# Optimization experiments

Hardware: AMD Instinct MI355X
Metric: run time of the kernel (lower is better)

## Reference

```python
import jax, jax.numpy as jnp
import numpy as np

N_NODES = 100000
N_EDGES = 1600000
IN_CH, HID_CH, OUT_CH = 128, 128, 64


def setup_inputs() -> dict:
    key = jax.random.key(0)
    k1, k2, k3, k4 = jax.random.split(key, 4)
    x = jax.random.normal(k1, (N_NODES, IN_CH), dtype=jnp.float32)
    edge_index = jax.random.randint(k2, (2, N_EDGES), 0, N_NODES, dtype=jnp.int64)
    # Glorot-like init for the two GCNConv weight matrices, zero biases (PyG default)
    W1 = jax.random.normal(k3, (IN_CH, HID_CH), dtype=jnp.float32) * (1.0 / np.sqrt(IN_CH))
    b1 = jnp.zeros((HID_CH,), dtype=jnp.float32)
    W2 = jax.random.normal(k4, (HID_CH, OUT_CH), dtype=jnp.float32) * (1.0 / np.sqrt(HID_CH))
    b2 = jnp.zeros((OUT_CH,), dtype=jnp.float32)
    return {"x": x, "edge_index": edge_index, "W1": W1, "b1": b1, "W2": W2, "b2": b2}


def _gcn_conv(x, src, dst, norm, W, b):
    """One GCNConv: linear transform, gather normalized source messages, scatter-add."""
    h = x @ W                                  # [N, out]
    msg = h[src] * norm[:, None]               # [E+N, out] gather + scale
    out = jax.ops.segment_sum(msg, dst, num_segments=N_NODES)  # scatter-add
    return out + b


def _build_norm(edge_index):
    # add self-loops (PyG GCNConv default add_self_loops=True)
    loops = jnp.arange(N_NODES, dtype=edge_index.dtype)
    src = jnp.concatenate([edge_index[0], loops])  # message sources (x_j)
    dst = jnp.concatenate([edge_index[1], loops])  # aggregation targets
    deg = jax.ops.segment_sum(jnp.ones_like(dst, dtype=jnp.float32), dst,
                              num_segments=N_NODES)
    dinv = jnp.where(deg > 0, jax.lax.rsqrt(jnp.maximum(deg, 1.0)), 0.0)
    norm = dinv[src] * dinv[dst]               # symmetric normalization per edge
    return src, dst, norm


def reference(x, edge_index, W1, b1, W2, b2):
    src, dst, norm = _build_norm(edge_index)
    h = _gcn_conv(x, src, dst, norm, W1, b1)
    h = jax.nn.relu(h)
    out = _gcn_conv(h, src, dst, norm, W2, b2)
    return out
```

## Files before the change

kernel.cpp:

```cpp
#include <hip/hip_runtime.h>
#include <cstdint>
#include <cstddef>

#define N_NODES 100000
#define N_EDGES 1600000
#define IN_CH   128
#define HID_CH  128
#define OUT_CH  64

#define AGG_BLOCKS 2048

#define SH    256
#define SHR   391
#define BCAP  7200
#define BK_CHUNK 4096
#define BK_NBLK ((N_EDGES + BK_CHUNK - 1) / BK_CHUNK)

__device__ __forceinline__ unsigned short f2bf(float f) {
    unsigned int u = __float_as_uint(f);
    unsigned int r = (u + 0x7FFFu + ((u >> 16) & 1u)) >> 16;
    return (unsigned short)r;
}
__device__ __forceinline__ float bfbits2f(unsigned int lo16) {
    return __uint_as_float(lo16 << 16);
}

typedef __attribute__((ext_vector_type(8))) short bf16x8;
typedef __attribute__((ext_vector_type(4))) float f32x4;

__global__ __launch_bounds__(512) void k_bucket(const int* __restrict__ ei,
                                                int* __restrict__ gcur,
                                                long long* __restrict__ buckets) {
    __shared__ int scount[8][SH];
    __shared__ int sbase[8][SH];
    const int tid  = threadIdx.x;
    const int w    = tid >> 6;
    const int base = blockIdx.x * BK_CHUNK;
    for (int i = tid; i < 8 * SH; i += 512) ((int*)scount)[i] = 0;
    __syncthreads();
    int dv[8], sv[8], shd[8], rk[8];
    #pragma unroll
    for (int k = 0; k < 8; k++) {
        int e = base + k * 512 + tid;
        if (e < N_EDGES) {
            dv[k] = __builtin_nontemporal_load(ei + N_EDGES + e);
            sv[k] = __builtin_nontemporal_load(ei + e);
            shd[k] = dv[k] / SHR;
            rk[k] = atomicAdd(&scount[w][shd[k]], 1);
        } else shd[k] = -1;
    }
    __syncthreads();
    if (tid < SH) {
        int c[8], tot = 0;
        #pragma unroll
        for (int q = 0; q < 8; q++) { c[q] = scount[q][tid]; tot += c[q]; }
        int run = atomicAdd(&gcur[tid], tot);
        #pragma unroll
        for (int q = 0; q < 8; q++) { sbase[q][tid] = run; run += c[q]; }
    }
    __syncthreads();
    #pragma unroll
    for (int k = 0; k < 8; k++) {
        if (shd[k] >= 0) {
            int pos = sbase[w][shd[k]] + rk[k];
            if (pos < BCAP)
                buckets[(size_t)shd[k] * BCAP + pos] =
                    ((long long)sv[k] << 32) | (unsigned int)dv[k];
        }
    }
}

__global__ __launch_bounds__(1024) void k_build(const long long* __restrict__ buckets,
                                                const int* __restrict__ gcur,
                                                int* __restrict__ rowptr,
                                                float* __restrict__ dinv,
                                                int* __restrict__ srcs) {
    __shared__ int hist[SHR];
    __shared__ int pref[SH];
    __shared__ int wsum[16];
    const int s  = blockIdx.x;
    const int lo = s * SHR;
    const int nb = min(SHR, N_NODES - lo);
    const int n  = min(gcur[s], BCAP);
    const int t = threadIdx.x, lane = t & 63, wid = t >> 6;
    const long long* bp = buckets + (size_t)s * BCAP;

    if (t < SH) pref[t] = gcur[t];
    for (int i = t; i < SHR; i += 1024) hist[i] = 0;
    __syncthreads();
    if (wid == 0) {
        int v0 = pref[lane * 4], v1 = pref[lane * 4 + 1];
        int v2 = pref[lane * 4 + 2], v3 = pref[lane * 4 + 3];
        int sl = v0 + v1 + v2 + v3;
        int x = sl;
        #pragma unroll
        for (int d = 1; d < 64; d <<= 1) {
            int y = __shfl_up(x, d, 64);
            if (lane >= d) x += y;
        }
        int excl = x - sl;
        pref[lane * 4]     = excl;
        pref[lane * 4 + 1] = excl + v0;
        pref[lane * 4 + 2] = excl + v0 + v1;
        pref[lane * 4 + 3] = excl + v0 + v1 + v2;
        if (s == 0 && lane == 63) rowptr[N_NODES] = x;
    }
    __syncthreads();
    const int gbase = pref[s];

    for (int i = t; i < n; i += 1024) {
        atomicAdd(&hist[(int)bp[i] - lo], 1);
    }
    __syncthreads();

    {
        int idx = t;
        int v = (idx < SHR) ? hist[idx] : 0;
        int x = v;
        #pragma unroll
        for (int d = 1; d < 64; d <<= 1) {
            int y = __shfl_up(x, d, 64);
            if (lane >= d) x += y;
        }
        if (lane == 63) wsum[wid] = x;
        __syncthreads();
        if (wid == 0) {
            int sv = (lane < 16) ? wsum[lane] : 0;
            #pragma unroll
            for (int d = 1; d < 16; d <<= 1) {
                int y = __shfl_up(sv, d, 64);
                if (lane >= d) sv += y;
            }
            if (lane < 16) wsum[lane] = sv;
        }
        __syncthreads();
        int woff = (wid == 0) ? 0 : wsum[wid - 1];
        int excl = woff + (x - v);
        if (idx < nb) {
            rowptr[lo + idx] = gbase + excl;
            dinv[lo + idx]   = rsqrtf((float)(v + 1));
        }
        if (idx < SHR) hist[idx] = excl;
        __syncthreads();
    }

    for (int i = t; i < n; i += 1024) {
        long long v = bp[i];
        int d  = (int)v;
        int sv = (int)(v >> 32);
        int pos = atomicAdd(&hist[d - lo], 1);
        srcs[gbase + pos] = sv;
    }
}

template <int OC>
__global__ __launch_bounds__(256) void k_gemm_mfma(const float* __restrict__ A,
                                                   const float* __restrict__ W,
                                                   unsigned short* __restrict__ hb) {
    __shared__ unsigned short As[128 * 128];
    __shared__ unsigned short Ws[OC * 128];
    const int tid = threadIdx.x;
    const int l   = tid & 63;
    const int wv  = tid >> 6;
    const int row0 = blockIdx.x * 128;

    #pragma unroll
    for (int it = 0; it < 16; it++) {
        int idx4 = it * 256 + tid;
        int r = idx4 >> 5, c4 = idx4 & 31;
        int gr = row0 + r; if (gr >= N_NODES) gr = N_NODES - 1;
        float4 v = ((const float4*)(A + (size_t)gr * 128))[c4];
        int bi = (r * 128 + c4 * 4) ^ ((r & 7) << 3);
        ushort4 pk;
        pk.x = f2bf(v.x); pk.y = f2bf(v.y); pk.z = f2bf(v.z); pk.w = f2bf(v.w);
        *(ushort4*)&As[bi] = pk;
    }
    for (int idx = tid; idx < 128 * OC; idx += 256) {
        int k = idx / OC, c = idx % OC;
        Ws[(c * 128 + k) ^ ((c & 7) << 3)] = f2bf(W[idx]);
    }
    __syncthreads();

    constexpr int NCF = OC / 16;
    f32x4 acc[2][NCF];
    #pragma unroll
    for (int a = 0; a < 2; a++)
        #pragma unroll
        for (int b = 0; b < NCF; b++) acc[a][b] = {0.f, 0.f, 0.f, 0.f};

    const int fr = l & 15;
    const int kg = (l >> 4) * 8;

    #pragma unroll
    for (int ks = 0; ks < 4; ks++) {
        const int kk = ks * 32 + kg;
        bf16x8 a0, a1;
        {
            int r = wv * 32 + fr;
            a0 = *(const bf16x8*)&As[(r * 128 + kk) ^ ((r & 7) << 3)];
            r += 16;
            a1 = *(const bf16x8*)&As[(r * 128 + kk) ^ ((r & 7) << 3)];
        }
        #pragma unroll
        for (int cf = 0; cf < NCF; cf++) {
            int c = cf * 16 + fr;
            bf16x8 b = *(const bf16x8*)&Ws[(c * 128 + kk) ^ ((c & 7) << 3)];
            acc[0][cf] = __builtin_amdgcn_mfma_f32_16x16x32_bf16(a0, b, acc[0][cf], 0, 0, 0);
            acc[1][cf] = __builtin_amdgcn_mfma_f32_16x16x32_bf16(a1, b, acc[1][cf], 0, 0, 0);
        }
    }

    const int g4 = (l >> 4) * 4;
    #pragma unroll
    for (int rf = 0; rf < 2; rf++)
        #pragma unroll
        for (int cf = 0; cf < NCF; cf++)
            #pragma unroll
            for (int r = 0; r < 4; r++) {
                int grow = row0 + wv * 32 + rf * 16 + g4 + r;
                if (grow < N_NODES)
                    hb[(size_t)grow * OC + cf * 16 + fr] = f2bf(acc[rf][cf][r]);
            }
}

template <int OC>
__global__ __launch_bounds__(256) void k_gemm_mfma_b(const unsigned short* __restrict__ A,
                                                     const float* __restrict__ W,
                                                     unsigned short* __restrict__ hb) {
    __shared__ unsigned short As[128 * 128];
    __shared__ unsigned short Ws[OC * 128];
    const int tid = threadIdx.x;
    const int l   = tid & 63;
    const int wv  = tid >> 6;
    const int row0 = blockIdx.x * 128;

    #pragma unroll
    for (int it = 0; it < 8; it++) {
        int idx8 = it * 256 + tid;
        int r = idx8 >> 4, c8 = idx8 & 15;
        int gr = row0 + r; if (gr >= N_NODES) gr = N_NODES - 1;
        uint4 v = ((const uint4*)(A + (size_t)gr * 128))[c8];
        int bi = (r * 128 + c8 * 8) ^ ((r & 7) << 3);
        *(uint4*)&As[bi] = v;
    }
    for (int idx = tid; idx < 128 * OC; idx += 256) {
        int k = idx / OC, c = idx % OC;
        Ws[(c * 128 + k) ^ ((c & 7) << 3)] = f2bf(W[idx]);
    }
    __syncthreads();

    constexpr int NCF = OC / 16;
    f32x4 acc[2][NCF];
    #pragma unroll
    for (int a = 0; a < 2; a++)
        #pragma unroll
        for (int b = 0; b < NCF; b++) acc[a][b] = {0.f, 0.f, 0.f, 0.f};

    const int fr = l & 15;
    const int kg = (l >> 4) * 8;

    #pragma unroll
    for (int ks = 0; ks < 4; ks++) {
        const int kk = ks * 32 + kg;
        bf16x8 a0, a1;
        {
            int r = wv * 32 + fr;
            a0 = *(const bf16x8*)&As[(r * 128 + kk) ^ ((r & 7) << 3)];
            r += 16;
            a1 = *(const bf16x8*)&As[(r * 128 + kk) ^ ((r & 7) << 3)];
        }
        #pragma unroll
        for (int cf = 0; cf < NCF; cf++) {
            int c = cf * 16 + fr;
            bf16x8 b = *(const bf16x8*)&Ws[(c * 128 + kk) ^ ((c & 7) << 3)];
            acc[0][cf] = __builtin_amdgcn_mfma_f32_16x16x32_bf16(a0, b, acc[0][cf], 0, 0, 0);
            acc[1][cf] = __builtin_amdgcn_mfma_f32_16x16x32_bf16(a1, b, acc[1][cf], 0, 0, 0);
        }
    }

    const int g4 = (l >> 4) * 4;
    #pragma unroll
    for (int rf = 0; rf < 2; rf++)
        #pragma unroll
        for (int cf = 0; cf < NCF; cf++)
            #pragma unroll
            for (int r = 0; r < 4; r++) {
                int grow = row0 + wv * 32 + rf * 16 + g4 + r;
                if (grow < N_NODES)
                    hb[(size_t)grow * OC + cf * 16 + fr] = f2bf(acc[rf][cf][r]);
            }
}

__global__ __launch_bounds__(256) void k_agg128bf(const unsigned int* __restrict__ hb,
                                                  const int* __restrict__ rowptr,
                                                  const int* __restrict__ srcs,
                                                  const float* __restrict__ dinv,
                                                  const float* __restrict__ bias,
                                                  unsigned int* __restrict__ outb,
                                                  int relu) {
    const int l = threadIdx.x & 63;
    const int wv0 = blockIdx.x * 4 + (threadIdx.x >> 6);
    const float2 bv = ((const float2*)bias)[l];

    for (int i = wv0; i < N_NODES; i += AGG_BLOCKS * 4) {
        const float di = dinv[i];
        unsigned int svv = hb[(size_t)i * 64 + l];
        const float sw = di * di;
        float2 acc;
        acc.x = bfbits2f(svv & 0xFFFFu) * sw;
        acc.y = bfbits2f(svv >> 16) * sw;

        const int start = rowptr[i], end = rowptr[i + 1];
        for (int b = start; b < end; b += 64) {
            const int eb = min(end - b, 64);
            int s = 0; float w = 0.f;
            if (l < eb) { s = srcs[b + l]; w = dinv[s] * di; }
            int j = 0;
            for (; j + 8 <= eb; j += 8) {
                int   si[8]; float wi[8];
                #pragma unroll
                for (int u = 0; u < 8; u++) { si[u] = __shfl(s, j + u); wi[u] = __shfl(w, j + u); }
                unsigned int v[8];
                #pragma unroll
                for (int u = 0; u < 8; u++) v[u] = hb[(size_t)si[u] * 64 + l];
                #pragma unroll
                for (int u = 0; u < 8; u++) {
                    acc.x = fmaf(bfbits2f(v[u] & 0xFFFFu), wi[u], acc.x);
                    acc.y = fmaf(bfbits2f(v[u] >> 16),     wi[u], acc.y);
                }
            }
            for (; j + 4 <= eb; j += 4) {
                int   si[4]; float wi[4];
                #pragma unroll
                for (int u = 0; u < 4; u++) { si[u] = __shfl(s, j + u); wi[u] = __shfl(w, j + u); }
                unsigned int v[4];
                #pragma unroll
                for (int u = 0; u < 4; u++) v[u] = hb[(size_t)si[u] * 64 + l];
                #pragma unroll
                for (int u = 0; u < 4; u++) {
                    acc.x = fmaf(bfbits2f(v[u] & 0xFFFFu), wi[u], acc.x);
                    acc.y = fmaf(bfbits2f(v[u] >> 16),     wi[u], acc.y);
                }
            }
            for (; j < eb; j++) {
                const int   sj = __shfl(s, j);
                const float wj = __shfl(w, j);
                unsigned int v = hb[(size_t)sj * 64 + l];
                acc.x = fmaf(bfbits2f(v & 0xFFFFu), wj, acc.x);
                acc.y = fmaf(bfbits2f(v >> 16),     wj, acc.y);
            }
        }
        acc.x += bv.x; acc.y += bv.y;
        if (relu) { acc.x = fmaxf(acc.x, 0.f); acc.y = fmaxf(acc.y, 0.f); }
        outb[(size_t)i * 64 + l] =
            (unsigned int)f2bf(acc.x) | ((unsigned int)f2bf(acc.y) << 16);
    }
}

__global__ __launch_bounds__(256) void k_agg64bf(const unsigned short* __restrict__ hb,
                                                 const int* __restrict__ rowptr,
                                                 const int* __restrict__ srcs,
                                                 const float* __restrict__ dinv,
                                                 const float* __restrict__ bias,
                                                 float* __restrict__ out,
                                                 int relu) {
    const int l = threadIdx.x & 63;
    const int wv0 = blockIdx.x * 4 + (threadIdx.x >> 6);
    const float bi = bias[l];

    for (int i = wv0; i < N_NODES; i += AGG_BLOCKS * 4) {
        const float di = dinv[i];
        float acc = bfbits2f((unsigned int)hb[(size_t)i * 64 + l]) * (di * di);

        const int start = rowptr[i], end = rowptr[i + 1];
        for (int b = start; b < end; b += 64) {
            const int eb = min(end - b, 64);
            int s = 0; float w = 0.f;
            if (l < eb) { s = srcs[b + l]; w = dinv[s] * di; }
            int j = 0;
            for (; j + 8 <= eb; j += 8) {
                int   si[8]; float wi[8];
                #pragma unroll
                for (int u = 0; u < 8; u++) { si[u] = __shfl(s, j + u); wi[u] = __shfl(w, j + u); }
                unsigned short v[8];
                #pragma unroll
                for (int u = 0; u < 8; u++) v[u] = hb[(size_t)si[u] * 64 + l];
                #pragma unroll
                for (int u = 0; u < 8; u++) acc = fmaf(bfbits2f((unsigned int)v[u]), wi[u], acc);
            }
            for (; j + 4 <= eb; j += 4) {
                int   si[4]; float wi[4];
                #pragma unroll
                for (int u = 0; u < 4; u++) { si[u] = __shfl(s, j + u); wi[u] = __shfl(w, j + u); }
                unsigned short v[4];
                #pragma unroll
                for (int u = 0; u < 4; u++) v[u] = hb[(size_t)si[u] * 64 + l];
                #pragma unroll
                for (int u = 0; u < 4; u++) acc = fmaf(bfbits2f((unsigned int)v[u]), wi[u], acc);
            }
            for (; j < eb; j++) {
                const int   sj = __shfl(s, j);
                const float wj = __shfl(w, j);
                acc = fmaf(bfbits2f((unsigned int)hb[(size_t)sj * 64 + l]), wj, acc);
            }
        }
        acc += bi;
        if (relu) acc = fmaxf(acc, 0.f);
        out[(size_t)i * 64 + l] = acc;
    }
}


extern "C" void kernel_launch(void* const* d_in, const int* in_sizes, int n_in,
                              void* d_out, int out_size, void* d_ws, size_t ws_size,
                              hipStream_t stream) {
    const float* x  = (const float*)d_in[0];
    const int*   ei = (const int*)d_in[1];
    const float* W1 = (const float*)d_in[2];
    const float* b1 = (const float*)d_in[3];
    const float* W2 = (const float*)d_in[4];
    const float* b2 = (const float*)d_in[5];
    float* out = (float*)d_out;

    char* p = (char*)d_ws;
    size_t used = 0;
    auto alloc = [&](size_t bytes) {
        void* q = (void*)p;
        size_t pad = (bytes + 255) & ~(size_t)255;
        p += pad;
        used += pad;
        return q;
    };
    int*   rowptr = (int*)alloc(sizeof(int) * (N_NODES + 1));
    float* dinv   = (float*)alloc(sizeof(float) * N_NODES);
    int*   gcur   = (int*)alloc(sizeof(int) * SH);
    int*   srcs   = (int*)alloc(sizeof(int) * N_EDGES);
    void*  regA   = alloc(sizeof(unsigned short) * (size_t)N_NODES * 128);
    long long* buckets = (long long*)regA;
    unsigned short* h1b = (unsigned short*)regA;
    unsigned int* agg1b = (unsigned int*)alloc(sizeof(unsigned int) * (size_t)N_NODES * 64);
    unsigned short* h2b = (unsigned short*)alloc(sizeof(unsigned short) * (size_t)N_NODES * 64);

    if (used > ws_size) return;

    hipMemsetAsync(gcur, 0, sizeof(int) * SH, stream);
    k_bucket<<<BK_NBLK, 512, 0, stream>>>(ei, gcur, buckets);
    k_build<<<SH, 1024, 0, stream>>>(buckets, gcur, rowptr, dinv, srcs);

    k_gemm_mfma<128><<<(N_NODES + 127) / 128, 256, 0, stream>>>(x, W1, h1b);
    k_agg128bf<<<AGG_BLOCKS, 256, 0, stream>>>((const unsigned int*)h1b, rowptr, srcs, dinv, b1, agg1b, 1);
    k_gemm_mfma_b<64><<<(N_NODES + 127) / 128, 256, 0, stream>>>((const unsigned short*)agg1b, W2, h2b);
    k_agg64bf<<<AGG_BLOCKS, 256, 0, stream>>>(h2b, rowptr, srcs, dinv, b2, out, 0);
}
```

Measured before the change: 194.4 us.

## Fuse bucketing with first GEMM and layer-1 aggregation with second GEMM

Edge bucketing and the first-layer GEMM now run as one horizontally fused launch, with block index choosing the role, so the two independent workloads overlap. Layer-1 aggregation (bias, ReLU) writes its 128-row tile straight into shared memory and feeds the second GEMM in the same block. This removes the agg1 intermediate round trip through global memory and two launches. In exchange, aggregation now uses only about 782 blocks with a fixed 32 nodes per wave instead of a 2048-block grid-stride loop, so load balance and occupancy may drop. Buckets also get their own buffer instead of aliasing h1b.

Result: slower. 276.9 us (+42.5%).

```diff
diff --git a/kernel.cpp b/kernel.cpp
--- a/kernel.cpp
+++ b/kernel.cpp
@@ -15,6 +15,7 @@
 #define BCAP  7200
 #define BK_CHUNK 4096
 #define BK_NBLK ((N_EDGES + BK_CHUNK - 1) / BK_CHUNK)
+#define GM_NBLK ((N_NODES + 127) / 128)
 
 __device__ __forceinline__ unsigned short f2bf(float f) {
     unsigned int u = __float_as_uint(f);
@@ -28,46 +29,106 @@
 typedef __attribute__((ext_vector_type(8))) short bf16x8;
 typedef __attribute__((ext_vector_type(4))) float f32x4;
 
-__global__ __launch_bounds__(512) void k_bucket(const int* __restrict__ ei,
+__global__ __launch_bounds__(512) void k_fused1(const int* __restrict__ ei,
                                                 int* __restrict__ gcur,
-                                                long long* __restrict__ buckets) {
-    __shared__ int scount[8][SH];
-    __shared__ int sbase[8][SH];
-    const int tid  = threadIdx.x;
-    const int w    = tid >> 6;
-    const int base = blockIdx.x * BK_CHUNK;
-    for (int i = tid; i < 8 * SH; i += 512) ((int*)scount)[i] = 0;
+                                                long long* __restrict__ buckets,
+                                                const float* __restrict__ A,
+                                                const float* __restrict__ W,
+                                                unsigned short* __restrict__ hb) {
+    __shared__ __align__(16) unsigned char smem[64 * 1024];
+    const int tid = threadIdx.x;
+
+    if (blockIdx.x < BK_NBLK) {
+        int (*scount)[SH] = (int(*)[SH])smem;
+        int (*sbase)[SH]  = (int(*)[SH])(smem + 8 * SH * 4);
+        const int w    = tid >> 6;
+        const int base = blockIdx.x * BK_CHUNK;
+        for (int i = tid; i < 8 * SH; i += 512) ((int*)scount)[i] = 0;
+        __syncthreads();
+        int dv[8], sv[8], shd[8], rk[8];
+        #pragma unroll
+        for (int k = 0; k < 8; k++) {
+            int e = base + k * 512 + tid;
+            if (e < N_EDGES) {
+                dv[k] = __builtin_nontemporal_load(ei + N_EDGES + e);
+                sv[k] = __builtin_nontemporal_load(ei + e);
+                shd[k] = dv[k] / SHR;
+                rk[k] = atomicAdd(&scount[w][shd[k]], 1);
+            } else shd[k] = -1;
+        }
+        __syncthreads();
+        if (tid < SH) {
+            int c[8], tot = 0;
+            #pragma unroll
+            for (int q = 0; q < 8; q++) { c[q] = scount[q][tid]; tot += c[q]; }
+            int run = atomicAdd(&gcur[tid], tot);
+            #pragma unroll
+            for (int q = 0; q < 8; q++) { sbase[q][tid] = run; run += c[q]; }
+        }
+        __syncthreads();
+        #pragma unroll
+        for (int k = 0; k < 8; k++) {
+            if (shd[k] >= 0) {
+                int pos = sbase[w][shd[k]] + rk[k];
+                if (pos < BCAP)
+                    buckets[(size_t)shd[k] * BCAP + pos] =
+                        ((long long)sv[k] << 32) | (unsigned int)dv[k];
+            }
+        }
+        return;
+    }
+
+    unsigned short* As = (unsigned short*)smem;
+    unsigned short* Ws = (unsigned short*)(smem + 32 * 1024);
+    const int l   = tid & 63;
+    const int wv  = tid >> 6;
+    const int row0 = (blockIdx.x - BK_NBLK) * 128;
+
+    #pragma unroll
+    for (int it = 0; it < 8; it++) {
+        int idx4 = it * 512 + tid;
+        int r = idx4 >> 5, c4 = idx4 & 31;
+        int gr = row0 + r; if (gr >= N_NODES) gr = N_NODES - 1;
+        float4 v = ((const float4*)(A + (size_t)gr * 128))[c4];
+        int bi = (r * 128 + c4 * 4) ^ ((r & 7) << 3);
+        ushort4 pk;
+        pk.x = f2bf(v.x); pk.y = f2bf(v.y); pk.z = f2bf(v.z); pk.w = f2bf(v.w);
+        *(ushort4*)&As[bi] = pk;
+    }
+    for (int idx = tid; idx < 128 * 128; idx += 512) {
+        int k = idx >> 7, c = idx & 127;
+        Ws[(c * 128 + k) ^ ((c & 7) << 3)] = f2bf(W[idx]);
+    }
     __syncthreads();
-    int dv[8], sv[8], shd[8], rk[8];
-    #pragma unroll
-    for (int k = 0; k < 8; k++) {
-        int e = base + k * 512 + tid;
-        if (e < N_EDGES) {
-            dv[k] = __builtin_nontemporal_load(ei + N_EDGES + e);
-            sv[k] = __builtin_nontemporal_load(ei + e);
-            shd[k] = dv[k] / SHR;
-            rk[k] = atomicAdd(&scount[w][shd[k]], 1);
-        } else shd[k] = -1;
-    }
-    __syncthreads();
-    if (tid < SH) {
-        int c[8], tot = 0;
-        #pragma unroll
-        for (int q = 0; q < 8; q++) { c[q] = scount[q][tid]; tot += c[q]; }
-        int run = atomicAdd(&gcur[tid], tot);
-        #pragma unroll
-        for (int q = 0; q < 8; q++) { sbase[q][tid] = run; run += c[q]; }
-    }
-    __syncthreads();
-    #pragma unroll
-    for (int k = 0; k < 8; k++) {
-        if (shd[k] >= 0) {
-            int pos = sbase[w][shd[k]] + rk[k];
-            if (pos < BCAP)
-                buckets[(size_t)shd[k] * BCAP + pos] =
-                    ((long long)sv[k] << 32) | (unsigned int)dv[k];
-        }
-    }
+
+    f32x4 acc[8];
+    #pragma unroll
+    for (int cf = 0; cf < 8; cf++) acc[cf] = {0.f, 0.f, 0.f, 0.f};
+    const int fr = l & 15;
+    const int kg = (l >> 4) * 8;
+
+    #pragma unroll
+    for (int ks = 0; ks < 4; ks++) {
+        const int kk = ks * 32 + kg;
+        int r = wv * 16 + fr;
+        bf16x8 a0 = *(const bf16x8*)&As[(r * 128 + kk) ^ ((r & 7) << 3)];
+        #pragma unroll
+        for (int cf = 0; cf < 8; cf++) {
+            int c = cf * 16 + fr;
+            bf16x8 b = *(const bf16x8*)&Ws[(c * 128 + kk) ^ ((c & 7) << 3)];
+            acc[cf] = __builtin_amdgcn_mfma_f32_16x16x32_bf16(a0, b, acc[cf], 0, 0, 0);
+        }
+    }
+
+    const int g4 = (l >> 4) * 4;
+    #pragma unroll
+    for (int cf = 0; cf < 8; cf++)
+        #pragma unroll
+        for (int r = 0; r < 4; r++) {
+            int grow = row0 + wv * 16 + g4 + r;
+            if (grow < N_NODES)
+                hb[(size_t)grow * 128 + cf * 16 + fr] = f2bf(acc[cf][r]);
+        }
 }
 
 __global__ __launch_bounds__(1024) void k_build(const long long* __restrict__ buckets,
@@ -153,44 +214,95 @@
     }
 }
 
-template <int OC>
-__global__ __launch_bounds__(256) void k_gemm_mfma(const float* __restrict__ A,
-                                                   const float* __restrict__ W,
-                                                   unsigned short* __restrict__ hb) {
-    __shared__ unsigned short As[128 * 128];
-    __shared__ unsigned short Ws[OC * 128];
+__global__ __launch_bounds__(256) void k_aggemm(const unsigned int* __restrict__ hb,
+                                                const int* __restrict__ rowptr,
+                                                const int* __restrict__ srcs,
+                                                const float* __restrict__ dinv,
+                                                const float* __restrict__ bias,
+                                                const float* __restrict__ W,
+                                                unsigned short* __restrict__ h2b) {
+    __shared__ __align__(16) unsigned char smem[48 * 1024];
+    unsigned short* As = (unsigned short*)smem;
+    unsigned short* Ws = (unsigned short*)(smem + 32 * 1024);
     const int tid = threadIdx.x;
     const int l   = tid & 63;
     const int wv  = tid >> 6;
     const int row0 = blockIdx.x * 128;
-
-    #pragma unroll
-    for (int it = 0; it < 16; it++) {
-        int idx4 = it * 256 + tid;
-        int r = idx4 >> 5, c4 = idx4 & 31;
-        int gr = row0 + r; if (gr >= N_NODES) gr = N_NODES - 1;
-        float4 v = ((const float4*)(A + (size_t)gr * 128))[c4];
-        int bi = (r * 128 + c4 * 4) ^ ((r & 7) << 3);
-        ushort4 pk;
-        pk.x = f2bf(v.x); pk.y = f2bf(v.y); pk.z = f2bf(v.z); pk.w = f2bf(v.w);
-        *(ushort4*)&As[bi] = pk;
-    }
-    for (int idx = tid; idx < 128 * OC; idx += 256) {
-        int k = idx / OC, c = idx % OC;
+    const float2 bv = ((const float2*)bias)[l];
+
+    for (int idx = tid; idx < 128 * 64; idx += 256) {
+        int k = idx >> 6, c = idx & 63;
         Ws[(c * 128 + k) ^ ((c & 7) << 3)] = f2bf(W[idx]);
     }
+
+    for (int t = 0; t < 32; t++) {
+        const int i = row0 + wv * 32 + t;
+        float2 acc = {0.f, 0.f};
+        if (i < N_NODES) {
+            const float di = dinv[i];
+            unsigned int svv = hb[(size_t)i * 64 + l];
+            const float sw = di * di;
+            acc.x = bfbits2f(svv & 0xFFFFu) * sw;
+            acc.y = bfbits2f(svv >> 16) * sw;
+
+            const int start = rowptr[i], end = rowptr[i + 1];
+            for (int b = start; b < end; b += 64) {
+                const int eb = min(end - b, 64);
+                int s = 0; float w = 0.f;
+                if (l < eb) { s = srcs[b + l]; w = dinv[s] * di; }
+                int j = 0;
+                for (; j + 8 <= eb; j += 8) {
+                    int   si[8]; float wi[8];
+                    #pragma unroll
+                    for (int u = 0; u < 8; u++) { si[u] = __shfl(s, j + u); wi[u] = __shfl(w, j + u); }
+                    unsigned int v[8];
+                    #pragma unroll
+                    for (int u = 0; u < 8; u++) v[u] = hb[(size_t)si[u] * 64 + l];
+                    #pragma unroll
+                    for (int u = 0; u < 8; u++) {
+                        acc.x = fmaf(bfbits2f(v[u] & 0xFFFFu), wi[u], acc.x);
+                        acc.y = fmaf(bfbits2f(v[u] >> 16),     wi[u], acc.y);
+                    }
+                }
+                for (; j + 4 <= eb; j += 4) {
+                    int   si[4]; float wi[4];
+                    #pragma unroll
+                    for (int u = 0; u < 4; u++) { si[u] = __shfl(s, j + u); wi[u] = __shfl(w, j + u); }
+                    unsigned int v[4];
+                    #pragma unroll
+                    for (int u = 0; u < 4; u++) v[u] = hb[(size_t)si[u] * 64 + l];
+                    #pragma unroll
+                    for (int u = 0; u < 4; u++) {
+                        acc.x = fmaf(bfbits2f(v[u] & 0xFFFFu), wi[u], acc.x);
+                        acc.y = fmaf(bfbits2f(v[u] >> 16),     wi[u], acc.y);
+                    }
+                }
+                for (; j < eb; j++) {
+                    const int   sj = __shfl(s, j);
+                    const float wj = __shfl(w, j);
+                    unsigned int v = hb[(size_t)sj * 64 + l];
+                    acc.x = fmaf(bfbits2f(v & 0xFFFFu), wj, acc.x);
+                    acc.y = fmaf(bfbits2f(v >> 16),     wj, acc.y);
+                }
+            }
+            acc.x = fmaxf(acc.x + bv.x, 0.f);
+            acc.y = fmaxf(acc.y + bv.y, 0.f);
+        }
+        const int r  = wv * 32 + t;
+        const int bi = (r * 128 + 2 * l) ^ ((r & 7) << 3);
+        *(unsigned int*)&As[bi] =
+            (unsigned int)f2bf(acc.x) | ((unsigned int)f2bf(acc.y) << 16);
+    }
     __syncthreads();
 
-    constexpr int NCF = OC / 16;
-    f32x4 acc[2][NCF];
+    f32x4 acc2[2][4];
     #pragma unroll
     for (int a = 0; a < 2; a++)
         #pragma unroll
-        for (int b = 0; b < NCF; b++) acc[a][b] = {0.f, 0.f, 0.f, 0.f};
+        for (int b = 0; b < 4; b++) acc2[a][b] = {0.f, 0.f, 0.f, 0.f};
 
     const int fr = l & 15;
     const int kg = (l >> 4) * 8;
-
     #pragma unroll
     for (int ks = 0; ks < 4; ks++) {
         const int kk = ks * 32 + kg;
@@ -202,11 +314,11 @@
             a1 = *(const bf16x8*)&As[(r * 128 + kk) ^ ((r & 7) << 3)];
         }
         #pragma unroll
-        for (int cf = 0; cf < NCF; cf++) {
+        for (int cf = 0; cf < 4; cf++) {
             int c = cf * 16 + fr;
             bf16x8 b = *(const bf16x8*)&Ws[(c * 128 + kk) ^ ((c & 7) << 3)];
-            acc[0][cf] = __builtin_amdgcn_mfma_f32_16x16x32_bf16(a0, b, acc[0][cf], 0, 0, 0);
-            acc[1][cf] = __builtin_amdgcn_mfma_f32_16x16x32_bf16(a1, b, acc[1][cf], 0, 0, 0);
+            acc2[0][cf] = __builtin_amdgcn_mfma_f32_16x16x32_bf16(a0, b, acc2[0][cf], 0, 0, 0);
+            acc2[1][cf] = __builtin_amdgcn_mfma_f32_16x16x32_bf16(a1, b, acc2[1][cf], 0, 0, 0);
         }
     }
 
@@ -214,147 +326,13 @@
     #pragma unroll
     for (int rf = 0; rf < 2; rf++)
         #pragma unroll
-        for (int cf = 0; cf < NCF; cf++)
+        for (int cf = 0; cf < 4; cf++)
             #pragma unroll
             for (int r = 0; r < 4; r++) {
                 int grow = row0 + wv * 32 + rf * 16 + g4 + r;
                 if (grow < N_NODES)
-                    hb[(size_t)grow * OC + cf * 16 + fr] = f2bf(acc[rf][cf][r]);
-            }
-}
-
-template <int OC>
-__global__ __launch_bounds__(256) void k_gemm_mfma_b(const unsigned short* __restrict__ A,
-                                                     const float* __restrict__ W,
-                                                     unsigned short* __restrict__ hb) {
-    __shared__ unsigned short As[128 * 128];
-    __shared__ unsigned short Ws[OC * 128];
-    const int tid = threadIdx.x;
-    const int l   = tid & 63;
-    const int wv  = tid >> 6;
-    const int row0 = blockIdx.x * 128;
-
-    #pragma unroll
-    for (int it = 0; it < 8; it++) {
-        int idx8 = it * 256 + tid;
-        int r = idx8 >> 4, c8 = idx8 & 15;
-        int gr = row0 + r; if (gr >= N_NODES) gr = N_NODES - 1;
-        uint4 v = ((const uint4*)(A + (size_t)gr * 128))[c8];
-        int bi = (r * 128 + c8 * 8) ^ ((r & 7) << 3);
-        *(uint4*)&As[bi] = v;
-    }
-    for (int idx = tid; idx < 128 * OC; idx += 256) {
-        int k = idx / OC, c = idx % OC;
-        Ws[(c * 128 + k) ^ ((c & 7) << 3)] = f2bf(W[idx]);
-    }
-    __syncthreads();
-
-    constexpr int NCF = OC / 16;
-    f32x4 acc[2][NCF];
-    #pragma unroll
-    for (int a = 0; a < 2; a++)
-        #pragma unroll
-        for (int b = 0; b < NCF; b++) acc[a][b] = {0.f, 0.f, 0.f, 0.f};
-
-    const int fr = l & 15;
-    const int kg = (l >> 4) * 8;
-
-    #pragma unroll
-    for (int ks = 0; ks < 4; ks++) {
-        const int kk = ks * 32 + kg;
-        bf16x8 a0, a1;
-        {
-            int r = wv * 32 + fr;
-            a0 = *(const bf16x8*)&As[(r * 128 + kk) ^ ((r & 7) << 3)];
-            r += 16;
-            a1 = *(const bf16x8*)&As[(r * 128 + kk) ^ ((r & 7) << 3)];
-        }
-        #pragma unroll
-        for (int cf = 0; cf < NCF; cf++) {
-            int c = cf * 16 + fr;
-            bf16x8 b = *(const bf16x8*)&Ws[(c * 128 + kk) ^ ((c & 7) << 3)];
-            acc[0][cf] = __builtin_amdgcn_mfma_f32_16x16x32_bf16(a0, b, acc[0][cf], 0, 0, 0);
-            acc[1][cf] = __builtin_amdgcn_mfma_f32_16x16x32_bf16(a1, b, acc[1][cf], 0, 0, 0);
-        }
-    }
-
-    const int g4 = (l >> 4) * 4;
-    #pragma unroll
-    for (int rf = 0; rf < 2; rf++)
-        #pragma unroll
-        for (int cf = 0; cf < NCF; cf++)
-            #pragma unroll
-            for (int r = 0; r < 4; r++) {
-                int grow = row0 + wv * 32 + rf * 16 + g4 + r;
-                if (grow < N_NODES)
-                    hb[(size_t)grow * OC + cf * 16 + fr] = f2bf(acc[rf][cf][r]);
-            }
-}
-
-__global__ __launch_bounds__(256) void k_agg128bf(const unsigned int* __restrict__ hb,
-                                                  const int* __restrict__ rowptr,
-                                                  const int* __restrict__ srcs,
-                                                  const float* __restrict__ dinv,
-                                                  const float* __restrict__ bias,
-                                                  unsigned int* __restrict__ outb,
-                                                  int relu) {
-    const int l = threadIdx.x & 63;
-    const int wv0 = blockIdx.x * 4 + (threadIdx.x >> 6);
-    const float2 bv = ((const float2*)bias)[l];
-
-    for (int i = wv0; i < N_NODES; i += AGG_BLOCKS * 4) {
-        const float di = dinv[i];
-        unsigned int svv = hb[(size_t)i * 64 + l];
-        const float sw = di * di;
-        float2 acc;
-        acc.x = bfbits2f(svv & 0xFFFFu) * sw;
-        acc.y = bfbits2f(svv >> 16) * sw;
-
-        const int start = rowptr[i], end = rowptr[i + 1];
-        for (int b = start; b < end; b += 64) {
-            const int eb = min(end - b, 64);
-            int s = 0; float w = 0.f;
-            if (l < eb) { s = srcs[b + l]; w = dinv[s] * di; }
-            int j = 0;
-            for (; j + 8 <= eb; j += 8) {
-                int   si[8]; float wi[8];
-                #pragma unroll
-                for (int u = 0; u < 8; u++) { si[u] = __shfl(s, j + u); wi[u] = __shfl(w, j + u); }
-                unsigned int v[8];
-                #pragma unroll
-                for (int u = 0; u < 8; u++) v[u] = hb[(size_t)si[u] * 64 + l];
-                #pragma unroll
-                for (int u = 0; u < 8; u++) {
-                    acc.x = fmaf(bfbits2f(v[u] & 0xFFFFu), wi[u], acc.x);
-                    acc.y = fmaf(bfbits2f(v[u] >> 16),     wi[u], acc.y);
-                }
-            }
-            for (; j + 4 <= eb; j += 4) {
-                int   si[4]; float wi[4];
-                #pragma unroll
-                for (int u = 0; u < 4; u++) { si[u] = __shfl(s, j + u); wi[u] = __shfl(w, j + u); }
-                unsigned int v[4];
-                #pragma unroll
-                for (int u = 0; u < 4; u++) v[u] = hb[(size_t)si[u] * 64 + l];
-                #pragma unroll
-                for (int u = 0; u < 4; u++) {
-                    acc.x = fmaf(bfbits2f(v[u] & 0xFFFFu), wi[u], acc.x);
-                    acc.y = fmaf(bfbits2f(v[u] >> 16),     wi[u], acc.y);
-                }
-            }
-            for (; j < eb; j++) {
-                const int   sj = __shfl(s, j);
-                const float wj = __shfl(w, j);
-                unsigned int v = hb[(size_t)sj * 64 + l];
-                acc.x = fmaf(bfbits2f(v & 0xFFFFu), wj, acc.x);
-                acc.y = fmaf(bfbits2f(v >> 16),     wj, acc.y);
-            }
-        }
-        acc.x += bv.x; acc.y += bv.y;
-        if (relu) { acc.x = fmaxf(acc.x, 0.f); acc.y = fmaxf(acc.y, 0.f); }
-        outb[(size_t)i * 64 + l] =
-            (unsigned int)f2bf(acc.x) | ((unsigned int)f2bf(acc.y) << 16);
-    }
+                    h2b[(size_t)grow * 64 + cf * 16 + fr] = f2bf(acc2[rf][cf][r]);
+            }
 }
 
 __global__ __launch_bounds__(256) void k_agg64bf(const unsigned short* __restrict__ hb,
@@ -435,20 +413,15 @@
     float* dinv   = (float*)alloc(sizeof(float) * N_NODES);
     int*   gcur   = (int*)alloc(sizeof(int) * SH);
     int*   srcs   = (int*)alloc(sizeof(int) * N_EDGES);
-    void*  regA   = alloc(sizeof(unsigned short) * (size_t)N_NODES * 128);
-    long long* buckets = (long long*)regA;
-    unsigned short* h1b = (unsigned short*)regA;
-    unsigned int* agg1b = (unsigned int*)alloc(sizeof(unsigned int) * (size_t)N_NODES * 64);
+    long long* buckets = (long long*)alloc(sizeof(long long) * (size_t)SH * BCAP);
+    unsigned short* h1b = (unsigned short*)alloc(sizeof(unsigned short) * (size_t)N_NODES * 128);
     unsigned short* h2b = (unsigned short*)alloc(sizeof(unsigned short) * (size_t)N_NODES * 64);
 
     if (used > ws_size) return;
 
     hipMemsetAsync(gcur, 0, sizeof(int) * SH, stream);
-    k_bucket<<<BK_NBLK, 512, 0, stream>>>(ei, gcur, buckets);
+    k_fused1<<<BK_NBLK + GM_NBLK, 512, 0, stream>>>(ei, gcur, buckets, x, W1, h1b);
     k_build<<<SH, 1024, 0, stream>>>(buckets, gcur, rowptr, dinv, srcs);
-
-    k_gemm_mfma<128><<<(N_NODES + 127) / 128, 256, 0, stream>>>(x, W1, h1b);
-    k_agg128bf<<<AGG_BLOCKS, 256, 0, stream>>>((const unsigned int*)h1b, rowptr, srcs, dinv, b1, agg1b, 1);
-    k_gemm_mfma_b<64><<<(N_NODES + 127) / 128, 256, 0, stream>>>((const unsigned short*)agg1b, W2, h2b);
+    k_aggemm<<<GM_NBLK, 256, 0, stream>>>((const unsigned int*)h1b, rowptr, srcs, dinv, b1, W2, h2b);
     k_agg64bf<<<AGG_BLOCKS, 256, 0, stream>>>(h2b, rowptr, srcs, dinv, b2, out, 0);
 }
```
